# Kernel tuning notes

Hardware: AMD Instinct MI355X
Metric: run time of the kernel (lower is better)

Reference implementation:

```python
import jax, jax.numpy as jnp
import numpy as np

N_NODES = 100000
N_EDGES = 1600000


def _gcn_layer(h, edge_row, edge_col, edge_val, W):
    # GraphConvolution (eval mode, dropout skipped):
    # support = h @ W ; out = spmm(adj, support)
    support = h @ W                                   # [N, d_out]
    msg = support[edge_col] * edge_val[:, None]       # [E, d_out] gather
    return jax.ops.segment_sum(msg, edge_row, num_segments=N_NODES)


def setup_inputs() -> dict:
    key = jax.random.key(0)
    ks = jax.random.split(key, 7)
    x = jax.random.normal(ks[0], (N_NODES, 256), dtype=jnp.float32)
    edge_row = jax.random.randint(ks[1], (N_EDGES,), 0, N_NODES, dtype=jnp.int32)
    edge_col = jax.random.randint(ks[2], (N_EDGES,), 0, N_NODES, dtype=jnp.int32)
    edge_val = jax.random.uniform(ks[3], (N_EDGES,), dtype=jnp.float32)
    W1 = jax.random.normal(ks[4], (256, 128), dtype=jnp.float32) * 0.05
    W2 = jax.random.normal(ks[5], (128, 64), dtype=jnp.float32) * 0.05
    W3 = jax.random.normal(ks[6], (128, 64), dtype=jnp.float32) * 0.05
    return {"x": x, "edge_row": edge_row, "edge_col": edge_col,
            "edge_val": edge_val, "W1": W1, "W2": W2, "W3": W3}


def reference(x, edge_row, edge_col, edge_val, W1, W2, W3):
    hidden1 = jax.nn.relu(_gcn_layer(x, edge_row, edge_col, edge_val, W1))
    mu = _gcn_layer(hidden1, edge_row, edge_col, edge_val, W2)      # act = identity
    logvar = _gcn_layer(hidden1, edge_row, edge_col, edge_val, W3)  # act = identity
    # reparameterize: z_mu = mean(mu); z_logvar = log(mean(exp(logvar)))
    z_mu = jnp.mean(mu)
    z_logvar = jnp.log(jnp.mean(jnp.exp(logvar)))
    return (z_mu, z_logvar)
```

## Files before the change

### kernel.cpp

```cpp
#include <hip/hip_runtime.h>
#include <cstdint>
#include <cstddef>

namespace {

constexpr int NN = 100000;
constexpr int NE = 1600000;
constexpr int DI = 256;
constexpr int DH = 128;
constexpr int DO = 64;
constexpr int SCAN_CHUNK = 1024;
constexpr int SCAN_NB = (NN + SCAN_CHUNK - 1) / SCAN_CHUNK;
constexpr int RANK_NB = NE / 256;
constexpr int EDOT_NB = NE / 256;
constexpr int SP3_NB = NN / 32;
constexpr int G1_NB = (NN + 127) / 128;
constexpr int PREP_NB = (DI * DH + DH * DO) / 256;

using bf16x8 = __attribute__((ext_vector_type(8))) short;
using f32x4  = __attribute__((ext_vector_type(4))) float;

__device__ inline unsigned short f2bf(float f) {
  unsigned int u = __float_as_uint(f);
  u += 0x7FFFu + ((u >> 16) & 1u);
  return (unsigned short)(u >> 16);
}
__device__ inline float bflo(unsigned int u) { return __uint_as_float(u << 16); }
__device__ inline float bfhi(unsigned int u) { return __uint_as_float(u & 0xffff0000u); }

__device__ inline void fma8(float* acc, const uint4 g, const float v) {
  acc[0] = fmaf(v, bflo(g.x), acc[0]); acc[1] = fmaf(v, bfhi(g.x), acc[1]);
  acc[2] = fmaf(v, bflo(g.y), acc[2]); acc[3] = fmaf(v, bfhi(g.y), acc[3]);
  acc[4] = fmaf(v, bflo(g.z), acc[4]); acc[5] = fmaf(v, bfhi(g.z), acc[5]);
  acc[6] = fmaf(v, bflo(g.w), acc[6]); acc[7] = fmaf(v, bfhi(g.w), acc[7]);
}

__device__ __forceinline__ void gl16(const void* g, void* l) {
  __builtin_amdgcn_global_load_lds(
      (const __attribute__((address_space(1))) void*)g,
      (__attribute__((address_space(3))) void*)l, 16, 0, 0);
}

__device__ __forceinline__ bf16x8 pack8(const f32x4 lo, const f32x4 hi) {
  bf16x8 r;
  r[0] = (short)f2bf(lo[0]); r[1] = (short)f2bf(lo[1]);
  r[2] = (short)f2bf(lo[2]); r[3] = (short)f2bf(lo[3]);
  r[4] = (short)f2bf(hi[0]); r[5] = (short)f2bf(hi[1]);
  r[6] = (short)f2bf(hi[2]); r[7] = (short)f2bf(hi[3]);
  return r;
}

template <int BM, int BN, int BK, bool ABF16>
__device__ __forceinline__ void gemm_block(const void* __restrict__ Ap,
                                           const unsigned short* __restrict__ Bt,
                                           unsigned short* __restrict__ C,
                                           int M, int K, int bx) {
  constexpr int ABYT = ABF16 ? 2 : 4;
  constexpr int SBA = BK * ABYT;
  constexpr int SBB = BK * 2;
  constexpr int ASZ = BM * SBA;
  constexpr int BSZ = BN * SBB;
  constexpr int OUTP = BN + 8;
  constexpr int OUTB = BM * OUTP * 2;
  constexpr int STAGE = ASZ + BSZ;
  constexpr int LDSB = STAGE > OUTB ? STAGE : OUTB;
  __shared__ __align__(16) char lds[LDSB];
  char* const as_ = lds;
  char* const bs_ = lds + ASZ;

  const int tid = threadIdx.x;
  const int wid = tid >> 6;
  const int lane = tid & 63;
  const int l15 = lane & 15;
  const int lg = lane >> 4;
  const int msk = (l15 & 7) << 4;
  const int row0 = bx * BM;

  constexpr int NGA = ASZ / (256 * 16);
  constexpr int NGB = BSZ / (256 * 16);
  const char* Ab = (const char*)Ap;
  const char* Bb = (const char*)Bt;

  f32x4 acc[2][BN / 16];
#pragma unroll
  for (int a = 0; a < 2; ++a)
#pragma unroll
    for (int b = 0; b < BN / 16; ++b) acc[a][b] = (f32x4)0.f;

  const int nk = K / BK;
  for (int t = 0; t < nk; ++t) {
    const int k0 = t * BK;
#pragma unroll
    for (int j = 0; j < NGA; ++j) {
      const int d = (j * 256 + tid) * 16;
      const int row = d / SBA;
      const int u = (d % SBA) ^ ((row & 7) << 4);
      int grow = row0 + row;
      if (grow >= M) grow = M - 1;
      gl16(Ab + (size_t)grow * (size_t)(K * ABYT) + k0 * ABYT + u, as_ + d);
    }
#pragma unroll
    for (int j = 0; j < NGB; ++j) {
      const int d = (j * 256 + tid) * 16;
      const int n = d / SBB;
      const int u = (d % SBB) ^ ((n & 7) << 4);
      gl16(Bb + (size_t)n * (size_t)(K * 2) + k0 * 2 + u, bs_ + d);
    }
    __syncthreads();
#pragma unroll
    for (int kk = 0; kk < BK; kk += 32) {
      const int koff = kk + lg * 8;
      bf16x8 a0, a1;
      if constexpr (!ABF16) {
        const int b0 = (wid * 32 + l15) * SBA + koff * 4;
        const int b1 = b0 + 16 * SBA;
        const f32x4 q00 = *(const f32x4*)(as_ + (b0 ^ msk));
        const f32x4 q01 = *(const f32x4*)(as_ + ((b0 ^ msk) ^ 16));
        const f32x4 q10 = *(const f32x4*)(as_ + (b1 ^ msk));
        const f32x4 q11 = *(const f32x4*)(as_ + ((b1 ^ msk) ^ 16));
        a0 = pack8(q00, q01);
        a1 = pack8(q10, q11);
      } else {
        const int b0 = (wid * 32 + l15) * SBA + koff * 2;
        const int b1 = b0 + 16 * SBA;
        a0 = *(const bf16x8*)(as_ + (b0 ^ msk));
        a1 = *(const bf16x8*)(as_ + (b1 ^ msk));
      }
#pragma unroll
      for (int nf = 0; nf < BN / 16; ++nf) {
        const int n = nf * 16 + l15;
        const bf16x8 b = *(const bf16x8*)(bs_ + ((n * SBB + koff * 2) ^ msk));
        acc[0][nf] = __builtin_amdgcn_mfma_f32_16x16x32_bf16(a0, b, acc[0][nf], 0, 0, 0);
        acc[1][nf] = __builtin_amdgcn_mfma_f32_16x16x32_bf16(a1, b, acc[1][nf], 0, 0, 0);
      }
    }
    __syncthreads();
  }
  unsigned short* outl = (unsigned short*)lds;
#pragma unroll
  for (int mf = 0; mf < 2; ++mf)
#pragma unroll
    for (int nf = 0; nf < BN / 16; ++nf)
#pragma unroll
      for (int r = 0; r < 4; ++r) {
        const int row = wid * 32 + mf * 16 + lg * 4 + r;
        const int col = nf * 16 + l15;
        outl[row * OUTP + col] = f2bf(acc[mf][nf][r]);
      }
  __syncthreads();
#pragma unroll
  for (int i = tid; i < BM * (BN / 8); i += 256) {
    const int m = i / (BN / 8), c8 = i % (BN / 8);
    const int row = row0 + m;
    if (row < M)
      *(float4*)(&C[(size_t)row * BN + c8 * 8]) = *(const float4*)(&outl[m * OUTP + c8 * 8]);
  }
}

__global__ __launch_bounds__(256) void k_prep(const float* __restrict__ W1,
                                              const float* __restrict__ W3,
                                              unsigned short* __restrict__ w1t,
                                              unsigned short* __restrict__ w3t) {
  const int i = blockIdx.x * 256 + threadIdx.x;
  if (i < DI * DH) {
    const int n = i / DI, k = i % DI;
    w1t[i] = f2bf(W1[k * DH + n]);
  } else {
    const int j = i - DI * DH;
    const int n = j / DH, k = j % DH;
    w3t[j] = f2bf(W3[k * DO + n]);
  }
}

__global__ __launch_bounds__(256) void k_g1_rank(const float* __restrict__ x,
                                                 const unsigned short* __restrict__ w1t,
                                                 unsigned short* __restrict__ sup,
                                                 const int* __restrict__ erow,
                                                 int* __restrict__ cnt,
                                                 int* __restrict__ rank) {
  const int b = blockIdx.x;
  if (b % 9 == 0) {
    gemm_block<128, 128, 64, false>(x, w1t, sup, NN, DI, b / 9);
  } else {
    const int rb = (b / 9) * 8 + (b % 9) - 1;
    if (rb < RANK_NB) {
      const int e = rb * 256 + threadIdx.x;
      rank[e] = atomicAdd(&cnt[erow[e]], 1);
    }
  }
}

__global__ __launch_bounds__(256) void k_g2_edot(const unsigned short* __restrict__ h1,
                                                 const unsigned short* __restrict__ w3t,
                                                 unsigned short* __restrict__ sup,
                                                 const int* __restrict__ ecol,
                                                 const float* __restrict__ eval,
                                                 const float* __restrict__ hw,
                                                 float* __restrict__ pzmu) {
  const int b = blockIdx.x;
  if (b % 9 == 0) {
    gemm_block<128, 64, 64, true>(h1, w3t, sup, NN, DH, b / 9);
  } else {
    const int eb = (b / 9) * 8 + (b % 9) - 1;
    if (eb < EDOT_NB) {
      __shared__ float red[256];
      const int i = eb * 256 + threadIdx.x;
      red[threadIdx.x] = eval[i] * hw[ecol[i]];
      __syncthreads();
      for (int off = 128; off > 0; off >>= 1) {
        if (threadIdx.x < off) red[threadIdx.x] += red[threadIdx.x + off];
        __syncthreads();
      }
      if (threadIdx.x == 0) pzmu[eb] = red[0];
    }
  }
}

__global__ __launch_bounds__(256) void k_scan1(const int* __restrict__ cnt,
                                               int* __restrict__ bsum) {
  __shared__ int red[256];
  const int b = blockIdx.x, t = threadIdx.x;
  const int base = b * SCAN_CHUNK + t * 4;
  int s = 0;
#pragma unroll
  for (int j = 0; j < 4; ++j) {
    const int idx = base + j;
    if (idx < NN) s += cnt[idx];
  }
  red[t] = s;
  __syncthreads();
  for (int off = 128; off > 0; off >>= 1) {
    if (t < off) red[t] += red[t + off];
    __syncthreads();
  }
  if (t == 0) bsum[b] = red[0];
}

__global__ __launch_bounds__(128) void k_scan2(const int* __restrict__ bsum,
                                               int* __restrict__ boff,
                                               int* __restrict__ rowptr) {
  __shared__ int s[128];
  const int t = threadIdx.x;
  const int v = (t < SCAN_NB) ? bsum[t] : 0;
  s[t] = v;
  __syncthreads();
  for (int off = 1; off < 128; off <<= 1) {
    int x = 0;
    if (t >= off) x = s[t - off];
    __syncthreads();
    s[t] += x;
    __syncthreads();
  }
  if (t < SCAN_NB) boff[t] = s[t] - v;
  if (t == 127) rowptr[NN] = s[127];
}

__global__ __launch_bounds__(256) void k_scan3(const int* __restrict__ cnt,
                                               const int* __restrict__ boff,
                                               int* __restrict__ rowptr) {
  __shared__ int tsum[256];
  const int b = blockIdx.x, t = threadIdx.x;
  const int base = b * SCAN_CHUNK + t * 4;
  int v[4];
#pragma unroll
  for (int j = 0; j < 4; ++j) {
    const int idx = base + j;
    v[j] = (idx < NN) ? cnt[idx] : 0;
  }
  const int pre1 = v[0];
  const int pre2 = pre1 + v[1];
  const int pre3 = pre2 + v[2];
  const int s = pre3 + v[3];
  tsum[t] = s;
  __syncthreads();
  for (int off = 1; off < 256; off <<= 1) {
    int x = 0;
    if (t >= off) x = tsum[t - off];
    __syncthreads();
    tsum[t] += x;
    __syncthreads();
  }
  const int excl = tsum[t] - s + boff[b];
  const int w[4] = {excl, excl + pre1, excl + pre2, excl + pre3};
#pragma unroll
  for (int j = 0; j < 4; ++j) {
    const int idx = base + j;
    if (idx < NN) rowptr[idx] = w[j];
  }
}

__global__ __launch_bounds__(256) void k_place_w2(
    const int* __restrict__ erow, const int* __restrict__ ecol,
    const float* __restrict__ eval, const int* __restrict__ rank,
    const int* __restrict__ rowptr, int2* __restrict__ cpk,
    const float* __restrict__ W2, float* __restrict__ w2s) {
  const int b = blockIdx.x;
  if (b < RANK_NB) {
    const int e = b * 256 + threadIdx.x;
    const int pos = rowptr[erow[e]] + rank[e];
    cpk[pos] = make_int2(ecol[e], __float_as_int(eval[e]));
  } else {
    const int k = threadIdx.x;
    if (k < DH) {
      float s = 0.f;
      for (int d = 0; d < DO; ++d) s += W2[k * DO + d];
      w2s[k] = s;
    }
  }
}

__global__ __launch_bounds__(256) void k_spmm1(const unsigned short* __restrict__ sup1,
                                               const int* __restrict__ rowptr,
                                               const int2* __restrict__ cpk,
                                               const float* __restrict__ w2s,
                                               unsigned short* __restrict__ h1,
                                               float* __restrict__ hw) {
  const int tid = threadIdx.x;
  const int lane = tid & 15;
  const int r = blockIdx.x * 16 + (tid >> 4);
  const int e0 = rowptr[r];
  const int e1 = rowptr[r + 1];
  const uint4* s8 = reinterpret_cast<const uint4*>(sup1);
  float aA[8] = {0,0,0,0,0,0,0,0}, aB[8] = {0,0,0,0,0,0,0,0};
  float aC[8] = {0,0,0,0,0,0,0,0}, aD[8] = {0,0,0,0,0,0,0,0};
  int e = e0;
  for (; e + 4 <= e1; e += 4) {
    const int2 p0 = cpk[e],     p1 = cpk[e + 1];
    const int2 p2 = cpk[e + 2], p3 = cpk[e + 3];
    const uint4 g0 = s8[(size_t)p0.x * 16 + lane];
    const uint4 g1 = s8[(size_t)p1.x * 16 + lane];
    const uint4 g2 = s8[(size_t)p2.x * 16 + lane];
    const uint4 g3 = s8[(size_t)p3.x * 16 + lane];
    fma8(aA, g0, __int_as_float(p0.y));
    fma8(aB, g1, __int_as_float(p1.y));
    fma8(aC, g2, __int_as_float(p2.y));
    fma8(aD, g3, __int_as_float(p3.y));
  }
  if (e + 2 <= e1) {
    const int2 p0 = cpk[e], p1 = cpk[e + 1];
    const uint4 g0 = s8[(size_t)p0.x * 16 + lane];
    const uint4 g1 = s8[(size_t)p1.x * 16 + lane];
    fma8(aA, g0, __int_as_float(p0.y));
    fma8(aB, g1, __int_as_float(p1.y));
    e += 2;
  }
  if (e < e1) {
    const int2 p0 = cpk[e];
    const uint4 g0 = s8[(size_t)p0.x * 16 + lane];
    fma8(aC, g0, __int_as_float(p0.y));
  }
  float acc[8];
#pragma unroll
  for (int j = 0; j < 8; ++j) acc[j] = fmaxf((aA[j] + aB[j]) + (aC[j] + aD[j]), 0.f);
  uint4 o;
  o.x = (unsigned)f2bf(acc[0]) | ((unsigned)f2bf(acc[1]) << 16);
  o.y = (unsigned)f2bf(acc[2]) | ((unsigned)f2bf(acc[3]) << 16);
  o.z = (unsigned)f2bf(acc[4]) | ((unsigned)f2bf(acc[5]) << 16);
  o.w = (unsigned)f2bf(acc[6]) | ((unsigned)f2bf(acc[7]) << 16);
  reinterpret_cast<uint4*>(h1)[(size_t)r * 16 + lane] = o;
  const float4 wlo = reinterpret_cast<const float4*>(w2s)[lane * 2];
  const float4 whi = reinterpret_cast<const float4*>(w2s)[lane * 2 + 1];
  float p = acc[0] * wlo.x + acc[1] * wlo.y + acc[2] * wlo.z + acc[3] * wlo.w +
            acc[4] * whi.x + acc[5] * whi.y + acc[6] * whi.z + acc[7] * whi.w;
#pragma unroll
  for (int off = 8; off > 0; off >>= 1) p += __shfl_down(p, off, 16);
  if (lane == 0) hw[r] = p;
}

__global__ __launch_bounds__(256) void k_spmm3(const unsigned short* __restrict__ sup3,
                                               const int* __restrict__ rowptr,
                                               const int2* __restrict__ cpk,
                                               float* __restrict__ pexp) {
  const int tid = threadIdx.x;
  const int lane = tid & 7;
  const int r = blockIdx.x * 32 + (tid >> 3);
  const int e0 = rowptr[r];
  const int e1 = rowptr[r + 1];
  const uint4* s8 = reinterpret_cast<const uint4*>(sup3);
  float aA[8] = {0,0,0,0,0,0,0,0}, aB[8] = {0,0,0,0,0,0,0,0};
  float aC[8] = {0,0,0,0,0,0,0,0}, aD[8] = {0,0,0,0,0,0,0,0};
  int e = e0;
  for (; e + 4 <= e1; e += 4) {
    const int2 p0 = cpk[e],     p1 = cpk[e + 1];
    const int2 p2 = cpk[e + 2], p3 = cpk[e + 3];
    const uint4 g0 = s8[(size_t)p0.x * 8 + lane];
    const uint4 g1 = s8[(size_t)p1.x * 8 + lane];
    const uint4 g2 = s8[(size_t)p2.x * 8 + lane];
    const uint4 g3 = s8[(size_t)p3.x * 8 + lane];
    fma8(aA, g0, __int_as_float(p0.y));
    fma8(aB, g1, __int_as_float(p1.y));
    fma8(aC, g2, __int_as_float(p2.y));
    fma8(aD, g3, __int_as_float(p3.y));
  }
  if (e + 2 <= e1) {
    const int2 p0 = cpk[e], p1 = cpk[e + 1];
    const uint4 g0 = s8[(size_t)p0.x * 8 + lane];
    const uint4 g1 = s8[(size_t)p1.x * 8 + lane];
    fma8(aA, g0, __int_as_float(p0.y));
    fma8(aB, g1, __int_as_float(p1.y));
    e += 2;
  }
  if (e < e1) {
    const int2 p0 = cpk[e];
    const uint4 g0 = s8[(size_t)p0.x * 8 + lane];
    fma8(aC, g0, __int_as_float(p0.y));
  }
  float p = 0.f;
#pragma unroll
  for (int j = 0; j < 8; ++j) p += expf((aA[j] + aB[j]) + (aC[j] + aD[j]));
#pragma unroll
  for (int off = 4; off > 0; off >>= 1) p += __shfl_down(p, off, 8);
  __shared__ float part[32];
  if (lane == 0) part[tid >> 3] = p;
  __syncthreads();
  if (tid == 0) {
    float s = 0.f;
#pragma unroll
    for (int i = 0; i < 32; ++i) s += part[i];
    pexp[blockIdx.x] = s;
  }
}

__global__ __launch_bounds__(256) void k_final(const float* __restrict__ pzmu, int nz,
                                               const float* __restrict__ pexp, int ne,
                                               float* __restrict__ out) {
  __shared__ float red[256];
  const int t = threadIdx.x;
  float s1 = 0.f, s2 = 0.f;
  for (int i = t; i < nz; i += 256) s1 += pzmu[i];
  for (int i = t; i < ne; i += 256) s2 += pexp[i];
  red[t] = s1;
  __syncthreads();
  for (int off = 128; off > 0; off >>= 1) {
    if (t < off) red[t] += red[t + off];
    __syncthreads();
  }
  const float tot1 = red[0];
  __syncthreads();
  red[t] = s2;
  __syncthreads();
  for (int off = 128; off > 0; off >>= 1) {
    if (t < off) red[t] += red[t + off];
    __syncthreads();
  }
  if (t == 0) {
    const float denom = (float)NN * (float)DO;
    out[0] = tot1 / denom;
    out[1] = logf(red[0] / denom);
  }
}

}

extern "C" void kernel_launch(void* const* d_in, const int* in_sizes, int n_in,
                              void* d_out, int out_size, void* d_ws, size_t ws_size,
                              hipStream_t stream) {
  const float* x    = (const float*)d_in[0];
  const int*   erow = (const int*)d_in[1];
  const int*   ecol = (const int*)d_in[2];
  const float* eval = (const float*)d_in[3];
  const float* W1   = (const float*)d_in[4];
  const float* W2   = (const float*)d_in[5];
  const float* W3   = (const float*)d_in[6];
  float* out = (float*)d_out;

  char* p = (char*)d_ws;
  auto alloc = [&](size_t bytes) -> void* {
    void* r = (void*)p;
    p += (bytes + 255) & ~(size_t)255;
    return r;
  };
  unsigned short* sup = (unsigned short*)alloc((size_t)NN * DH * 2);
  unsigned short* h1  = (unsigned short*)alloc((size_t)NN * DH * 2);
  int2*  cpk    = (int2*)alloc((size_t)NE * 8);
  int*   rank   = (int*)alloc((size_t)NE * 4);
  int*   rowptr = (int*)alloc((size_t)(NN + 1) * 4);
  int*   cnt    = (int*)alloc((size_t)NN * 4);
  float* hw     = (float*)alloc((size_t)NN * 4);
  float* w2s    = (float*)alloc(DH * 4);
  unsigned short* w1t = (unsigned short*)alloc((size_t)DH * DI * 2);
  unsigned short* w3t = (unsigned short*)alloc((size_t)DO * DH * 2);
  int*   bsum   = (int*)alloc(SCAN_NB * 4);
  int*   boff   = (int*)alloc(SCAN_NB * 4);
  float* pexp   = (float*)alloc(SP3_NB * 4);
  float* pzmu   = (float*)alloc(EDOT_NB * 4);

  hipMemsetAsync(cnt, 0, (size_t)NN * 4, stream);

  k_prep<<<PREP_NB, 256, 0, stream>>>(W1, W3, w1t, w3t);

  k_g1_rank<<<G1_NB * 9, 256, 0, stream>>>(x, w1t, sup, erow, cnt, rank);

  k_scan1<<<SCAN_NB, 256, 0, stream>>>(cnt, bsum);
  k_scan2<<<1, 128, 0, stream>>>(bsum, boff, rowptr);
  k_scan3<<<SCAN_NB, 256, 0, stream>>>(cnt, boff, rowptr);

  k_place_w2<<<RANK_NB + 1, 256, 0, stream>>>(erow, ecol, eval, rank, rowptr, cpk, W2, w2s);

  k_spmm1<<<NN / 16, 256, 0, stream>>>(sup, rowptr, cpk, w2s, h1, hw);

  k_g2_edot<<<G1_NB * 9, 256, 0, stream>>>(h1, w3t, sup, ecol, eval, hw, pzmu);

  k_spmm3<<<NN / 32, 256, 0, stream>>>(sup, rowptr, cpk, pexp);

  k_final<<<1, 256, 0, stream>>>(pzmu, EDOT_NB, pexp, SP3_NB, out);
}
```

Measured before the change: 235.3 us.

## Fuse first SpMM with second GEMM via LDS tile, merge spmm3 with edge-dot

The first-layer SpMM now runs per 128-row block, keeps the ReLU'd hidden tile in swizzled shared memory, and immediately multiplies it by W3 with MFMA, writing only the 64-wide support. This removes the h1 write/read round trip and one kernel launch. The edge-dot reduction for z_mu moves into the spmm3 launch as extra blocks. In exchange the fused kernel uses 32KB of LDS and launches only ~782 blocks, each doing 8 serial row groups, which lowers occupancy and parallelism for the gather phase.

```diff
diff --git a/kernel.cpp b/kernel.cpp
--- a/kernel.cpp
+++ b/kernel.cpp
@@ -190,32 +190,6 @@
   }
 }
 
-__global__ __launch_bounds__(256) void k_g2_edot(const unsigned short* __restrict__ h1,
-                                                 const unsigned short* __restrict__ w3t,
-                                                 unsigned short* __restrict__ sup,
-                                                 const int* __restrict__ ecol,
-                                                 const float* __restrict__ eval,
-                                                 const float* __restrict__ hw,
-                                                 float* __restrict__ pzmu) {
-  const int b = blockIdx.x;
-  if (b % 9 == 0) {
-    gemm_block<128, 64, 64, true>(h1, w3t, sup, NN, DH, b / 9);
-  } else {
-    const int eb = (b / 9) * 8 + (b % 9) - 1;
-    if (eb < EDOT_NB) {
-      __shared__ float red[256];
-      const int i = eb * 256 + threadIdx.x;
-      red[threadIdx.x] = eval[i] * hw[ecol[i]];
-      __syncthreads();
-      for (int off = 128; off > 0; off >>= 1) {
-        if (threadIdx.x < off) red[threadIdx.x] += red[threadIdx.x + off];
-        __syncthreads();
-      }
-      if (threadIdx.x == 0) pzmu[eb] = red[0];
-    }
-  }
-}
-
 __global__ __launch_bounds__(256) void k_scan1(const int* __restrict__ cnt,
                                                int* __restrict__ bsum) {
   __shared__ int red[256];
@@ -309,115 +283,191 @@
   }
 }
 
-__global__ __launch_bounds__(256) void k_spmm1(const unsigned short* __restrict__ sup1,
-                                               const int* __restrict__ rowptr,
-                                               const int2* __restrict__ cpk,
-                                               const float* __restrict__ w2s,
-                                               unsigned short* __restrict__ h1,
-                                               float* __restrict__ hw) {
+__global__ __launch_bounds__(256) void k_spmm1_g2(
+    const unsigned short* __restrict__ sup1,
+    const int* __restrict__ rowptr,
+    const int2* __restrict__ cpk,
+    const float* __restrict__ w2s,
+    const unsigned short* __restrict__ w3t,
+    unsigned short* __restrict__ sup3,
+    float* __restrict__ hw) {
+  __shared__ __align__(16) unsigned short hl[128 * 128];
   const int tid = threadIdx.x;
-  const int lane = tid & 15;
-  const int r = blockIdx.x * 16 + (tid >> 4);
-  const int e0 = rowptr[r];
-  const int e1 = rowptr[r + 1];
+  const int lane16 = tid & 15;
+  const int row0 = blockIdx.x * 128;
   const uint4* s8 = reinterpret_cast<const uint4*>(sup1);
-  float aA[8] = {0,0,0,0,0,0,0,0}, aB[8] = {0,0,0,0,0,0,0,0};
-  float aC[8] = {0,0,0,0,0,0,0,0}, aD[8] = {0,0,0,0,0,0,0,0};
-  int e = e0;
-  for (; e + 4 <= e1; e += 4) {
-    const int2 p0 = cpk[e],     p1 = cpk[e + 1];
-    const int2 p2 = cpk[e + 2], p3 = cpk[e + 3];
-    const uint4 g0 = s8[(size_t)p0.x * 16 + lane];
-    const uint4 g1 = s8[(size_t)p1.x * 16 + lane];
-    const uint4 g2 = s8[(size_t)p2.x * 16 + lane];
-    const uint4 g3 = s8[(size_t)p3.x * 16 + lane];
-    fma8(aA, g0, __int_as_float(p0.y));
-    fma8(aB, g1, __int_as_float(p1.y));
-    fma8(aC, g2, __int_as_float(p2.y));
-    fma8(aD, g3, __int_as_float(p3.y));
-  }
-  if (e + 2 <= e1) {
-    const int2 p0 = cpk[e], p1 = cpk[e + 1];
-    const uint4 g0 = s8[(size_t)p0.x * 16 + lane];
-    const uint4 g1 = s8[(size_t)p1.x * 16 + lane];
-    fma8(aA, g0, __int_as_float(p0.y));
-    fma8(aB, g1, __int_as_float(p1.y));
-    e += 2;
-  }
-  if (e < e1) {
-    const int2 p0 = cpk[e];
-    const uint4 g0 = s8[(size_t)p0.x * 16 + lane];
-    fma8(aC, g0, __int_as_float(p0.y));
-  }
-  float acc[8];
-#pragma unroll
-  for (int j = 0; j < 8; ++j) acc[j] = fmaxf((aA[j] + aB[j]) + (aC[j] + aD[j]), 0.f);
-  uint4 o;
-  o.x = (unsigned)f2bf(acc[0]) | ((unsigned)f2bf(acc[1]) << 16);
-  o.y = (unsigned)f2bf(acc[2]) | ((unsigned)f2bf(acc[3]) << 16);
-  o.z = (unsigned)f2bf(acc[4]) | ((unsigned)f2bf(acc[5]) << 16);
-  o.w = (unsigned)f2bf(acc[6]) | ((unsigned)f2bf(acc[7]) << 16);
-  reinterpret_cast<uint4*>(h1)[(size_t)r * 16 + lane] = o;
-  const float4 wlo = reinterpret_cast<const float4*>(w2s)[lane * 2];
-  const float4 whi = reinterpret_cast<const float4*>(w2s)[lane * 2 + 1];
-  float p = acc[0] * wlo.x + acc[1] * wlo.y + acc[2] * wlo.z + acc[3] * wlo.w +
-            acc[4] * whi.x + acc[5] * whi.y + acc[6] * whi.z + acc[7] * whi.w;
-#pragma unroll
-  for (int off = 8; off > 0; off >>= 1) p += __shfl_down(p, off, 16);
-  if (lane == 0) hw[r] = p;
-}
-
-__global__ __launch_bounds__(256) void k_spmm3(const unsigned short* __restrict__ sup3,
-                                               const int* __restrict__ rowptr,
-                                               const int2* __restrict__ cpk,
-                                               float* __restrict__ pexp) {
-  const int tid = threadIdx.x;
-  const int lane = tid & 7;
-  const int r = blockIdx.x * 32 + (tid >> 3);
-  const int e0 = rowptr[r];
-  const int e1 = rowptr[r + 1];
-  const uint4* s8 = reinterpret_cast<const uint4*>(sup3);
-  float aA[8] = {0,0,0,0,0,0,0,0}, aB[8] = {0,0,0,0,0,0,0,0};
-  float aC[8] = {0,0,0,0,0,0,0,0}, aD[8] = {0,0,0,0,0,0,0,0};
-  int e = e0;
-  for (; e + 4 <= e1; e += 4) {
-    const int2 p0 = cpk[e],     p1 = cpk[e + 1];
-    const int2 p2 = cpk[e + 2], p3 = cpk[e + 3];
-    const uint4 g0 = s8[(size_t)p0.x * 8 + lane];
-    const uint4 g1 = s8[(size_t)p1.x * 8 + lane];
-    const uint4 g2 = s8[(size_t)p2.x * 8 + lane];
-    const uint4 g3 = s8[(size_t)p3.x * 8 + lane];
-    fma8(aA, g0, __int_as_float(p0.y));
-    fma8(aB, g1, __int_as_float(p1.y));
-    fma8(aC, g2, __int_as_float(p2.y));
-    fma8(aD, g3, __int_as_float(p3.y));
-  }
-  if (e + 2 <= e1) {
-    const int2 p0 = cpk[e], p1 = cpk[e + 1];
-    const uint4 g0 = s8[(size_t)p0.x * 8 + lane];
-    const uint4 g1 = s8[(size_t)p1.x * 8 + lane];
-    fma8(aA, g0, __int_as_float(p0.y));
-    fma8(aB, g1, __int_as_float(p1.y));
-    e += 2;
-  }
-  if (e < e1) {
-    const int2 p0 = cpk[e];
-    const uint4 g0 = s8[(size_t)p0.x * 8 + lane];
-    fma8(aC, g0, __int_as_float(p0.y));
-  }
-  float p = 0.f;
-#pragma unroll
-  for (int j = 0; j < 8; ++j) p += expf((aA[j] + aB[j]) + (aC[j] + aD[j]));
-#pragma unroll
-  for (int off = 4; off > 0; off >>= 1) p += __shfl_down(p, off, 8);
-  __shared__ float part[32];
-  if (lane == 0) part[tid >> 3] = p;
-  __syncthreads();
-  if (tid == 0) {
-    float s = 0.f;
-#pragma unroll
-    for (int i = 0; i < 32; ++i) s += part[i];
-    pexp[blockIdx.x] = s;
+
+  const float4 wlo = reinterpret_cast<const float4*>(w2s)[lane16 * 2];
+  const float4 whi = reinterpret_cast<const float4*>(w2s)[lane16 * 2 + 1];
+#pragma unroll 1
+  for (int pg = 0; pg < 8; ++pg) {
+    const int rloc = pg * 16 + (tid >> 4);
+    const int r = row0 + rloc;
+    const int rr = r < NN ? r : NN - 1;
+    const int e0 = rowptr[rr];
+    const int e1 = rowptr[rr + 1];
+    float aA[8] = {0,0,0,0,0,0,0,0}, aB[8] = {0,0,0,0,0,0,0,0};
+    float aC[8] = {0,0,0,0,0,0,0,0}, aD[8] = {0,0,0,0,0,0,0,0};
+    int e = e0;
+    for (; e + 4 <= e1; e += 4) {
+      const int2 p0 = cpk[e],     p1 = cpk[e + 1];
+      const int2 p2 = cpk[e + 2], p3 = cpk[e + 3];
+      const uint4 g0 = s8[(size_t)p0.x * 16 + lane16];
+      const uint4 g1 = s8[(size_t)p1.x * 16 + lane16];
+      const uint4 g2 = s8[(size_t)p2.x * 16 + lane16];
+      const uint4 g3 = s8[(size_t)p3.x * 16 + lane16];
+      fma8(aA, g0, __int_as_float(p0.y));
+      fma8(aB, g1, __int_as_float(p1.y));
+      fma8(aC, g2, __int_as_float(p2.y));
+      fma8(aD, g3, __int_as_float(p3.y));
+    }
+    if (e + 2 <= e1) {
+      const int2 p0 = cpk[e], p1 = cpk[e + 1];
+      const uint4 g0 = s8[(size_t)p0.x * 16 + lane16];
+      const uint4 g1 = s8[(size_t)p1.x * 16 + lane16];
+      fma8(aA, g0, __int_as_float(p0.y));
+      fma8(aB, g1, __int_as_float(p1.y));
+      e += 2;
+    }
+    if (e < e1) {
+      const int2 p0 = cpk[e];
+      const uint4 g0 = s8[(size_t)p0.x * 16 + lane16];
+      fma8(aC, g0, __int_as_float(p0.y));
+    }
+    float acc[8];
+#pragma unroll
+    for (int j = 0; j < 8; ++j) acc[j] = fmaxf((aA[j] + aB[j]) + (aC[j] + aD[j]), 0.f);
+    uint4 o;
+    o.x = (unsigned)f2bf(acc[0]) | ((unsigned)f2bf(acc[1]) << 16);
+    o.y = (unsigned)f2bf(acc[2]) | ((unsigned)f2bf(acc[3]) << 16);
+    o.z = (unsigned)f2bf(acc[4]) | ((unsigned)f2bf(acc[5]) << 16);
+    o.w = (unsigned)f2bf(acc[6]) | ((unsigned)f2bf(acc[7]) << 16);
+    const int byte = (rloc * 256 + lane16 * 16) ^ ((rloc & 7) << 4);
+    *(uint4*)((char*)hl + byte) = o;
+    float pd = acc[0] * wlo.x + acc[1] * wlo.y + acc[2] * wlo.z + acc[3] * wlo.w +
+               acc[4] * whi.x + acc[5] * whi.y + acc[6] * whi.z + acc[7] * whi.w;
+#pragma unroll
+    for (int off = 8; off > 0; off >>= 1) pd += __shfl_down(pd, off, 16);
+    if (lane16 == 0 && r < NN) hw[r] = pd;
+  }
+  __syncthreads();
+
+  const int wid = tid >> 6;
+  const int lane = tid & 63;
+  const int l15 = lane & 15;
+  const int lg = lane >> 4;
+  const int msk = (l15 & 7) << 4;
+  f32x4 acc2[2][4];
+#pragma unroll
+  for (int a = 0; a < 2; ++a)
+#pragma unroll
+    for (int b = 0; b < 4; ++b) acc2[a][b] = (f32x4)0.f;
+#pragma unroll
+  for (int kk = 0; kk < 128; kk += 32) {
+    const int koff = kk + lg * 8;
+    const int b0 = (wid * 32 + l15) * 256 + koff * 2;
+    const int b1 = b0 + 16 * 256;
+    const bf16x8 a0 = *(const bf16x8*)((char*)hl + (b0 ^ msk));
+    const bf16x8 a1 = *(const bf16x8*)((char*)hl + (b1 ^ msk));
+#pragma unroll
+    for (int nf = 0; nf < 4; ++nf) {
+      const int n = nf * 16 + l15;
+      const bf16x8 b = *(const bf16x8*)(&w3t[n * 128 + koff]);
+      acc2[0][nf] = __builtin_amdgcn_mfma_f32_16x16x32_bf16(a0, b, acc2[0][nf], 0, 0, 0);
+      acc2[1][nf] = __builtin_amdgcn_mfma_f32_16x16x32_bf16(a1, b, acc2[1][nf], 0, 0, 0);
+    }
+  }
+  __syncthreads();
+  unsigned short* outl = hl;
+#pragma unroll
+  for (int mf = 0; mf < 2; ++mf)
+#pragma unroll
+    for (int nf = 0; nf < 4; ++nf)
+#pragma unroll
+      for (int r = 0; r < 4; ++r) {
+        const int row = wid * 32 + mf * 16 + lg * 4 + r;
+        const int col = nf * 16 + l15;
+        outl[row * 72 + col] = f2bf(acc2[mf][nf][r]);
+      }
+  __syncthreads();
+#pragma unroll
+  for (int i = tid; i < 128 * 8; i += 256) {
+    const int m = i / 8, c8 = i % 8;
+    const int row = row0 + m;
+    if (row < NN)
+      *(float4*)(&sup3[(size_t)row * 64 + c8 * 8]) = *(const float4*)(&outl[m * 72 + c8 * 8]);
+  }
+}
+
+__global__ __launch_bounds__(256) void k_spmm3_edot(
+    const unsigned short* __restrict__ sup3,
+    const int* __restrict__ rowptr,
+    const int2* __restrict__ cpk,
+    const int* __restrict__ ecol,
+    const float* __restrict__ eval,
+    const float* __restrict__ hw,
+    float* __restrict__ pexp,
+    float* __restrict__ pzmu) {
+  if (blockIdx.x < SP3_NB) {
+    const int tid = threadIdx.x;
+    const int lane = tid & 7;
+    const int r = blockIdx.x * 32 + (tid >> 3);
+    const int e0 = rowptr[r];
+    const int e1 = rowptr[r + 1];
+    const uint4* s8 = reinterpret_cast<const uint4*>(sup3);
+    float aA[8] = {0,0,0,0,0,0,0,0}, aB[8] = {0,0,0,0,0,0,0,0};
+    float aC[8] = {0,0,0,0,0,0,0,0}, aD[8] = {0,0,0,0,0,0,0,0};
+    int e = e0;
+    for (; e + 4 <= e1; e += 4) {
+      const int2 p0 = cpk[e],     p1 = cpk[e + 1];
+      const int2 p2 = cpk[e + 2], p3 = cpk[e + 3];
+      const uint4 g0 = s8[(size_t)p0.x * 8 + lane];
+      const uint4 g1 = s8[(size_t)p1.x * 8 + lane];
+      const uint4 g2 = s8[(size_t)p2.x * 8 + lane];
+      const uint4 g3 = s8[(size_t)p3.x * 8 + lane];
+      fma8(aA, g0, __int_as_float(p0.y));
+      fma8(aB, g1, __int_as_float(p1.y));
+      fma8(aC, g2, __int_as_float(p2.y));
+      fma8(aD, g3, __int_as_float(p3.y));
+    }
+    if (e + 2 <= e1) {
+      const int2 p0 = cpk[e], p1 = cpk[e + 1];
+      const uint4 g0 = s8[(size_t)p0.x * 8 + lane];
+      const uint4 g1 = s8[(size_t)p1.x * 8 + lane];
+      fma8(aA, g0, __int_as_float(p0.y));
+      fma8(aB, g1, __int_as_float(p1.y));
+      e += 2;
+    }
+    if (e < e1) {
+      const int2 p0 = cpk[e];
+      const uint4 g0 = s8[(size_t)p0.x * 8 + lane];
+      fma8(aC, g0, __int_as_float(p0.y));
+    }
+    float p = 0.f;
+#pragma unroll
+    for (int j = 0; j < 8; ++j) p += expf((aA[j] + aB[j]) + (aC[j] + aD[j]));
+#pragma unroll
+    for (int off = 4; off > 0; off >>= 1) p += __shfl_down(p, off, 8);
+    __shared__ float part[32];
+    if (lane == 0) part[tid >> 3] = p;
+    __syncthreads();
+    if (tid == 0) {
+      float s = 0.f;
+#pragma unroll
+      for (int i = 0; i < 32; ++i) s += part[i];
+      pexp[blockIdx.x] = s;
+    }
+  } else {
+    const int b = blockIdx.x - SP3_NB;
+    const int i = b * 256 + threadIdx.x;
+    __shared__ float red[256];
+    red[threadIdx.x] = eval[i] * hw[ecol[i]];
+    __syncthreads();
+    for (int off = 128; off > 0; off >>= 1) {
+      if (threadIdx.x < off) red[threadIdx.x] += red[threadIdx.x + off];
+      __syncthreads();
+    }
+    if (threadIdx.x == 0) pzmu[b] = red[0];
   }
 }
 
@@ -470,8 +520,8 @@
     p += (bytes + 255) & ~(size_t)255;
     return r;
   };
-  unsigned short* sup = (unsigned short*)alloc((size_t)NN * DH * 2);
-  unsigned short* h1  = (unsigned short*)alloc((size_t)NN * DH * 2);
+  unsigned short* sup  = (unsigned short*)alloc((size_t)NN * DH * 2);
+  unsigned short* sup3 = (unsigned short*)alloc((size_t)NN * DO * 2);
   int2*  cpk    = (int2*)alloc((size_t)NE * 8);
   int*   rank   = (int*)alloc((size_t)NE * 4);
   int*   rowptr = (int*)alloc((size_t)(NN + 1) * 4);
@@ -497,11 +547,10 @@
 
   k_place_w2<<<RANK_NB + 1, 256, 0, stream>>>(erow, ecol, eval, rank, rowptr, cpk, W2, w2s);
 
-  k_spmm1<<<NN / 16, 256, 0, stream>>>(sup, rowptr, cpk, w2s, h1, hw);
-
-  k_g2_edot<<<G1_NB * 9, 256, 0, stream>>>(h1, w3t, sup, ecol, eval, hw, pzmu);
-
-  k_spmm3<<<NN / 32, 256, 0, stream>>>(sup, rowptr, cpk, pexp);
+  k_spmm1_g2<<<G1_NB, 256, 0, stream>>>(sup, rowptr, cpk, w2s, w3t, sup3, hw);
+
+  k_spmm3_edot<<<SP3_NB + EDOT_NB, 256, 0, stream>>>(sup3, rowptr, cpk, ecol, eval, hw,
+                                                     pexp, pzmu);
 
   k_final<<<1, 256, 0, stream>>>(pzmu, EDOT_NB, pexp, SP3_NB, out);
 }
```

New measurement: 269.0 us. 1.14x slower.
